# Performance work log

Measured on AMD Instinct MI355X. Metric: run time of the kernel, lower is better.

## Reference

```python
import jax, jax.numpy as jnp
import numpy as np

N = 30000          # nodes
DEG = 16           # in-degree per node
E = N * DEG        # edges per etype
T = 3              # edge types
IN = 128           # in_feats
HID = 256          # hidden_size
HEADS = 4
CLS = 2            # num_classes
NEG_SLOPE = 0.2    # DGL GATConv default


def setup_inputs() -> dict:
    key = jax.random.key(0)
    ks = jax.random.split(key, 14)
    s = lambda k, shape: (jax.random.normal(k, shape, jnp.float32) * 0.05)
    feat = jax.random.normal(ks[0], (N, IN), jnp.float32)
    src = jax.random.randint(ks[1], (T, E), 0, N)
    # every node gets exactly DEG incoming edges per etype (DGL forbids 0-in-degree)
    dst = jnp.tile(jnp.repeat(jnp.arange(N), DEG), (T, 1))
    D = HID // HEADS
    return {
        "feat": feat,
        "W0": s(ks[2], (T, IN, HID)),  "al0": s(ks[3], (T, HEADS, D)), "ar0": s(ks[4], (T, HEADS, D)), "b0": jnp.zeros((T, HID), jnp.float32),
        "W1": s(ks[5], (T, HID, HID)), "al1": s(ks[6], (T, HEADS, D)), "ar1": s(ks[7], (T, HEADS, D)), "b1": jnp.zeros((T, HID), jnp.float32),
        "W2": s(ks[8], (T, HID, CLS)), "al2": s(ks[9], (T, 1, CLS)),   "ar2": s(ks[10], (T, 1, CLS)), "b2": jnp.zeros((T, CLS), jnp.float32),
        "src": src, "dst": dst,
    }


def _gat(feat, W, al, ar, b, src, dst):
    """DGL GATConv: feat [n,F], W [F,H*D], al/ar [H,D], b [H*D] -> [n,H,D]."""
    n = feat.shape[0]
    H, D = al.shape
    h = (feat @ W).reshape(n, H, D)                      # projected features
    el = jnp.sum(h * al, axis=-1)                        # [n,H]
    er = jnp.sum(h * ar, axis=-1)                        # [n,H]
    e = jax.nn.leaky_relu(el[src] + er[dst], NEG_SLOPE)  # [E,H] edge scores
    # segment softmax over incoming edges of each dst node
    emax = jax.ops.segment_max(e, dst, num_segments=n)
    ex = jnp.exp(e - emax[dst])
    den = jax.ops.segment_sum(ex, dst, num_segments=n)
    alpha = ex / den[dst]                                # [E,H]
    out = jax.ops.segment_sum(h[src] * alpha[:, :, None], dst, num_segments=n)
    return out + b.reshape(H, D)


def _hetero(feat, W, al, ar, b, src, dst):
    # HeteroGraphConv(aggregate='mean') over T edge types on one node type
    outs = [_gat(feat, W[t], al[t], ar[t], b[t], src[t], dst[t]) for t in range(W.shape[0])]
    return jnp.mean(jnp.stack(outs, 0), axis=0)


def reference(feat, W0, al0, ar0, b0, W1, al1, ar1, b1, W2, al2, ar2, b2, src, dst):
    h = jax.nn.elu(_hetero(feat, W0, al0, ar0, b0, src, dst).reshape(N, -1))
    h = jax.nn.elu(_hetero(h, W1, al1, ar1, b1, src, dst).reshape(N, -1))
    logits = _hetero(h, W2, al2, ar2, b2, src, dst)      # [N,1,CLS]
    # faithful to F.softmax(logits[primary_ntype], dim=1): dim=1 is the size-1 head axis
    return logits, jax.nn.softmax(logits, axis=1)
```

## Files before the change

kernel.cpp:

```cpp
#include <hip/hip_runtime.h>
#include <hip/hip_bf16.h>
#include <hip/hip_fp8.h>
#include <math.h>

#define N_NODES 30000
#define DEG     16
#define NE      480000
#define NT      3
#define IN_F    128
#define HID_F   256
#define HEADS   4
#define DH      64
#define CLS     2
#define SLOPE   0.2f

#define NTILES      1875
#define NTILES_AL   1880
#define KC0         4
#define KC1         8

typedef __hip_bfloat16 bf16;
typedef __attribute__((ext_vector_type(8))) short short8;
typedef __attribute__((ext_vector_type(4))) float floatx4;
typedef __attribute__((ext_vector_type(2))) float f32x2;

__device__ __forceinline__ float bf2f(short x) {
    unsigned int u = ((unsigned int)(unsigned short)x) << 16;
    float f;
    __builtin_memcpy(&f, &u, 4);
    return f;
}
__device__ __forceinline__ short f2bf_s(float x) {
    bf16 b = bf16(x);
    short s;
    __builtin_memcpy(&s, &b, 2);
    return s;
}

__device__ __forceinline__ void gload_lds16(const void* g, void* l) {
    __builtin_amdgcn_global_load_lds(
        (const __attribute__((address_space(1))) unsigned int*)g,
        (__attribute__((address_space(3))) unsigned int*)l, 16, 0, 0);
}

__device__ __forceinline__ f32x2 fp8_lo(unsigned int u) {
#if __has_builtin(__builtin_amdgcn_cvt_pk_f32_fp8)
    return __builtin_amdgcn_cvt_pk_f32_fp8((int)u, false);
#else
    __hip_fp8_e4m3 q0, q1;
    q0.__x = (unsigned char)(u & 0xff);
    q1.__x = (unsigned char)((u >> 8) & 0xff);
    return (f32x2){(float)q0, (float)q1};
#endif
}
__device__ __forceinline__ f32x2 fp8_hi(unsigned int u) {
#if __has_builtin(__builtin_amdgcn_cvt_pk_f32_fp8)
    return __builtin_amdgcn_cvt_pk_f32_fp8((int)u, true);
#else
    __hip_fp8_e4m3 q2, q3;
    q2.__x = (unsigned char)((u >> 16) & 0xff);
    q3.__x = (unsigned char)((u >> 24) & 0xff);
    return (f32x2){(float)q2, (float)q3};
#endif
}
__device__ __forceinline__ unsigned int fp8_encode4_u32(float v0, float v1,
                                                        float v2, float v3) {
#if __has_builtin(__builtin_amdgcn_cvt_pk_fp8_f32)
    int p01 = __builtin_amdgcn_cvt_pk_fp8_f32(v0, v1, 0, false);
    int p23 = __builtin_amdgcn_cvt_pk_fp8_f32(v2, v3, 0, false);
    return ((unsigned int)p01 & 0xffffu) | ((unsigned int)p23 << 16);
#else
    __hip_fp8_e4m3 q0(v0), q1(v1), q2(v2), q3(v3);
    return (unsigned int)q0.__x | ((unsigned int)q1.__x << 8) |
           ((unsigned int)q2.__x << 16) | ((unsigned int)q3.__x << 24);
#endif
}


#define APACK_THREADS (N_NODES * (IN_F / 8))
#define BP0_THREADS   (NT * 16 * KC0 * 64)
#define BP1_THREADS   (NT * 16 * KC1 * 64)
__global__ void prep(const float* __restrict__ feat, const float* __restrict__ W0,
                     const float* __restrict__ W1, short* __restrict__ Apack0,
                     short* __restrict__ Bpack0, short* __restrict__ Bpack1) {
    int g = blockIdx.x * 256 + threadIdx.x;
    if (g < APACK_THREADS) {
        int row = g >> 4, j8 = g & 15;
        int k0 = j8 * 8;
        const float* src = feat + (size_t)row * IN_F + k0;
        int ntile = row >> 4, C = k0 >> 5, quad = (k0 >> 3) & 3;
        int lane  = (row & 15) + 16 * quad;
        short* dst = Apack0 + ((size_t)(ntile * KC0 + C) * 64 + lane) * 8;
        short8 o;
#pragma unroll
        for (int j = 0; j < 8; j++) o[j] = f2bf_s(src[j]);
        *(short8*)dst = o;
        return;
    }
    g -= APACK_THREADS;
    if (g < BP0_THREADS) {
        int t = g / (16 * KC0 * 64), rem = g % (16 * KC0 * 64);
        int nt = rem / (KC0 * 64);
        int C  = (rem / 64) % KC0;
        int lane = rem & 63, l15 = lane & 15, quad = lane >> 4;
        int col = nt * 16 + l15, k0 = C * 32 + quad * 8;
        const float* src = W0 + (size_t)t * IN_F * HID_F + (size_t)k0 * HID_F + col;
        short* dst = Bpack0 + ((size_t)t * 16 * KC0 + nt * KC0 + C) * 512 + lane * 8;
        short8 o;
#pragma unroll
        for (int j = 0; j < 8; j++) o[j] = f2bf_s(src[(size_t)j * HID_F]);
        *(short8*)dst = o;
        return;
    }
    g -= BP0_THREADS;
    if (g < BP1_THREADS) {
        int t = g / (16 * KC1 * 64), rem = g % (16 * KC1 * 64);
        int nt = rem / (KC1 * 64);
        int C  = (rem / 64) % KC1;
        int lane = rem & 63, l15 = lane & 15, quad = lane >> 4;
        int col = nt * 16 + l15, k0 = C * 32 + quad * 8;
        const float* src = W1 + (size_t)t * HID_F * HID_F + (size_t)k0 * HID_F + col;
        short* dst = Bpack1 + ((size_t)t * 16 * KC1 + nt * KC1 + C) * 512 + lane * 8;
        short8 o;
#pragma unroll
        for (int j = 0; j < 8; j++) o[j] = f2bf_s(src[(size_t)j * HID_F]);
        *(short8*)dst = o;
    }
}

template <int K>
__global__ __launch_bounds__(256, 4) void gemm_proj(const short* __restrict__ Apack,
                                                    const short* __restrict__ Bpack,
                                                    const float* __restrict__ al,
                                                    const float* __restrict__ ar,
                                                    unsigned char* __restrict__ Hout,
                                                    float* __restrict__ el,
                                                    float* __restrict__ er) {
    const int KC = K / 32;
    int nh   = blockIdx.y;
    int t    = blockIdx.z;
    int tid  = threadIdx.x;
    int wave = tid >> 6, lane = tid & 63;
    int quad = lane >> 4, l15 = lane & 15;
    int e0   = blockIdx.x * 8 + wave * 2;

    __shared__ __align__(16) unsigned char Blds[4 * KC * 1024];

    {
        const short* Bp_panel = Bpack + ((size_t)t * 16 + nh * 4) * KC * 512;
#pragma unroll
        for (int i = 0; i < KC; i++) {
            int chunk = wave + i * 4;
            gload_lds16(Bp_panel + (size_t)chunk * 512 + lane * 8,
                        Blds + chunk * 1024);
        }
    }

    const short* Ap0 = Apack + (size_t)(e0)     * KC * 512 + lane * 8;
    const short* Ap1 = Apack + (size_t)(e0 + 1) * KC * 512 + lane * 8;
    unsigned char* Ht = Hout + (size_t)t * N_NODES * HID_F;

    floatx4 acc[4][2];
#pragma unroll
    for (int i = 0; i < 4; i++) {
        acc[i][0] = (floatx4){0.f, 0.f, 0.f, 0.f};
        acc[i][1] = (floatx4){0.f, 0.f, 0.f, 0.f};
    }

    asm volatile("s_waitcnt vmcnt(0)" ::: "memory");
    __syncthreads();

#pragma unroll
    for (int C = 0; C < KC; C++) {
        short8 xb0 = *(const short8*)(Ap0 + (size_t)C * 512);
        short8 xb1 = *(const short8*)(Ap1 + (size_t)C * 512);
#pragma unroll
        for (int nt = 0; nt < 4; nt++) {
            short8 wa = *(const short8*)(Blds + (size_t)(nt * KC + C) * 1024 + lane * 16);
            acc[nt][0] = __builtin_amdgcn_mfma_f32_16x16x32_bf16(wa, xb0, acc[nt][0], 0, 0, 0);
            acc[nt][1] = __builtin_amdgcn_mfma_f32_16x16x32_bf16(wa, xb1, acc[nt][1], 0, 0, 0);
        }
    }

#pragma unroll
    for (int e = 0; e < 2; e++) {
        int node = (e0 + e) * 16 + l15;
        bool ok  = node < N_NODES;
#pragma unroll
        for (int nt = 0; nt < 4; nt++) {
            unsigned int u = fp8_encode4_u32(acc[nt][e][0], acc[nt][e][1],
                                             acc[nt][e][2], acc[nt][e][3]);
            if (ok)
                *(unsigned int*)(Ht + (size_t)node * HID_F + (nh * 4 + nt) * 16 + quad * 4) = u;
        }
        {
            float pl = 0.f, pr = 0.f;
#pragma unroll
            for (int nt = 0; nt < 4; nt++) {
                int coff = t * HID_F + (nh * 4 + nt) * 16 + quad * 4;
                float4 av = *(const float4*)(al + coff);
                float4 rv = *(const float4*)(ar + coff);
                pl += acc[nt][e][0] * av.x + acc[nt][e][1] * av.y +
                      acc[nt][e][2] * av.z + acc[nt][e][3] * av.w;
                pr += acc[nt][e][0] * rv.x + acc[nt][e][1] * rv.y +
                      acc[nt][e][2] * rv.z + acc[nt][e][3] * rv.w;
            }
            pl += __shfl_xor(pl, 16); pl += __shfl_xor(pl, 32);
            pr += __shfl_xor(pr, 16); pr += __shfl_xor(pr, 32);
            if (lane < 16 && ok) {
                el[((size_t)t * N_NODES + node) * HEADS + nh] = pl;
                er[((size_t)t * N_NODES + node) * HEADS + nh] = pr;
            }
        }
    }
}

template <bool PACK>
__global__ __launch_bounds__(256, 8) void gat_agg(const unsigned char* __restrict__ Hproj,
                                                  const float* __restrict__ el,
                                                  const float* __restrict__ er,
                                                  const int* __restrict__ src,
                                                  const float* __restrict__ bias,
                                                  short* __restrict__ out) {
    int blk = blockIdx.x;
    int tid = threadIdx.x;
    __shared__ __align__(16) int   s_src[16][NT][DEG];
    __shared__ __align__(16) float s_w[16][NT][HEADS][DEG];

#pragma unroll
    for (int t = 0; t < NT; t++) {
        int j = tid;
        s_src[j >> 4][t][j & 15] = src[(size_t)t * NE + blk * 256 + j];
    }
    __syncthreads();

    {
        int lane16 = tid & 15;
        int ubase  = tid >> 4;
#pragma unroll
        for (int it = 0; it < 12; it++) {
            int u = it * 16 + ubase;
            int g = u / 12, rem = u % 12;
            int t = rem >> 2, h = rem & 3;
            int n = blk * 16 + g;
            int s = s_src[g][t][lane16];
            float e = el[((size_t)t * N_NODES + s) * HEADS + h] +
                      er[((size_t)t * N_NODES + n) * HEADS + h];
            e = e > 0.f ? e : SLOPE * e;
            float m = e;
            m = fmaxf(m, __shfl_xor(m, 1));
            m = fmaxf(m, __shfl_xor(m, 2));
            m = fmaxf(m, __shfl_xor(m, 4));
            m = fmaxf(m, __shfl_xor(m, 8));
            float p = __expf(e - m);
            float ss = p;
            ss += __shfl_xor(ss, 1);
            ss += __shfl_xor(ss, 2);
            ss += __shfl_xor(ss, 4);
            ss += __shfl_xor(ss, 8);
            s_w[g][t][h][lane16] = p / ss;
        }
    }
    __syncthreads();

    int g = tid >> 4, c = tid & 15;
    int n = blk * 16 + g;
    int h = c >> 2;
    int col0 = c * 16;

    f32x2 acc2[8];
#pragma unroll
    for (int k = 0; k < 8; k++) acc2[k] = (f32x2){0.f, 0.f};

    const uint4* Hb = (const uint4*)Hproj;
    unsigned cu = (unsigned)c;

#pragma unroll
    for (int t = 0; t < NT; t++) {
        const unsigned tb = (unsigned)t * (N_NODES * 16u);
        const float* wp = s_w[g][t][h];
#pragma unroll
        for (int half = 0; half < 2; half++) {
            uint4 v[8];
#pragma unroll
            for (int i = 0; i < 8; i++) {
                int s = s_src[g][t][half * 8 + i];
                v[i] = Hb[tb + (unsigned)s * 16u + cu];
            }
#pragma unroll
            for (int i = 0; i < 8; i++) {
                float wsc = wp[half * 8 + i];
                f32x2 w2 = (f32x2){wsc, wsc};
                acc2[0] += w2 * fp8_lo(v[i].x);
                acc2[1] += w2 * fp8_hi(v[i].x);
                acc2[2] += w2 * fp8_lo(v[i].y);
                acc2[3] += w2 * fp8_hi(v[i].y);
                acc2[4] += w2 * fp8_lo(v[i].z);
                acc2[5] += w2 * fp8_hi(v[i].z);
                acc2[6] += w2 * fp8_lo(v[i].w);
                acc2[7] += w2 * fp8_hi(v[i].w);
            }
        }
    }

    short8 o0, o1;
#pragma unroll
    for (int j = 0; j < 8; j++) {
        float av = acc2[j >> 1][j & 1];
        float bsum = bias[0 * HID_F + col0 + j] + bias[1 * HID_F + col0 + j] +
                     bias[2 * HID_F + col0 + j];
        float res = (av + bsum) * (1.f / 3.f);
        res = res > 0.f ? res : (__expf(res) - 1.f);
        o0[j] = f2bf_s(res);
    }
#pragma unroll
    for (int j = 0; j < 8; j++) {
        float av = acc2[4 + (j >> 1)][j & 1];
        int cj = col0 + 8 + j;
        float bsum = bias[0 * HID_F + cj] + bias[1 * HID_F + cj] +
                     bias[2 * HID_F + cj];
        float res = (av + bsum) * (1.f / 3.f);
        res = res > 0.f ? res : (__expf(res) - 1.f);
        o1[j] = f2bf_s(res);
    }
    if (PACK) {
        int C = c >> 1;
        int lane0 = g + 16 * ((2 * c) & 3);
        int lane1 = g + 16 * ((2 * c + 1) & 3);
        *(short8*)(out + ((size_t)(blk * KC1 + C) * 64 + lane0) * 8) = o0;
        *(short8*)(out + ((size_t)(blk * KC1 + C) * 64 + lane1) * 8) = o1;
    } else {
        *(short8*)(out + (size_t)n * HID_F + col0) = o0;
        *(short8*)(out + (size_t)n * HID_F + col0 + 8) = o1;
    }
}

__global__ __launch_bounds__(256) void proj2(const short* __restrict__ X,
                                             const float* __restrict__ W2,
                                             const float* __restrict__ al2,
                                             const float* __restrict__ ar2,
                                             float* __restrict__ p2,
                                             float* __restrict__ el2,
                                             float* __restrict__ er2) {
    int n    = blockIdx.x * 4 + (threadIdx.x >> 6);
    int lane = threadIdx.x & 63;
    const short* Xr = X + (size_t)n * HID_F + lane * 4;
    float x[4];
    x[0] = bf2f(Xr[0]); x[1] = bf2f(Xr[1]); x[2] = bf2f(Xr[2]); x[3] = bf2f(Xr[3]);
    float a[NT][CLS];
#pragma unroll
    for (int t = 0; t < NT; t++)
#pragma unroll
        for (int cc = 0; cc < CLS; cc++) {
            float v = 0.f;
#pragma unroll
            for (int j = 0; j < 4; j++)
                v += x[j] * W2[(size_t)t * HID_F * CLS + (lane * 4 + j) * CLS + cc];
#pragma unroll
            for (int off = 32; off; off >>= 1) v += __shfl_xor(v, off);
            a[t][cc] = v;
        }
    if (lane == 0) {
#pragma unroll
        for (int t = 0; t < NT; t++) {
            p2[((size_t)t * N_NODES + n) * CLS + 0] = a[t][0];
            p2[((size_t)t * N_NODES + n) * CLS + 1] = a[t][1];
            el2[(size_t)t * N_NODES + n] = a[t][0] * al2[t * CLS + 0] + a[t][1] * al2[t * CLS + 1];
            er2[(size_t)t * N_NODES + n] = a[t][0] * ar2[t * CLS + 0] + a[t][1] * ar2[t * CLS + 1];
        }
    }
}

__global__ void final_layer(const float* __restrict__ p2,
                            const float* __restrict__ el2,
                            const float* __restrict__ er2,
                            const int* __restrict__ src,
                            const float* __restrict__ b2,
                            float* __restrict__ out) {
    int n = blockIdx.x * 256 + threadIdx.x;
    if (n >= N_NODES) return;
    float l0 = 0.f, l1 = 0.f;
    for (int t = 0; t < NT; t++) {
        float erv = er2[(size_t)t * N_NODES + n];
        const int* sp = src + (size_t)t * NE + n * DEG;
        float ev[DEG];
        float m = -1e30f;
#pragma unroll
        for (int i = 0; i < DEG; i++) {
            int s   = sp[i];
            float e = el2[(size_t)t * N_NODES + s] + erv;
            e = e > 0.f ? e : SLOPE * e;
            ev[i] = e;
            m = fmaxf(m, e);
        }
        float den = 0.f, a0 = 0.f, a1 = 0.f;
#pragma unroll
        for (int i = 0; i < DEG; i++) {
            int s   = sp[i];
            float p = __expf(ev[i] - m);
            den += p;
            a0  += p * p2[((size_t)t * N_NODES + s) * CLS + 0];
            a1  += p * p2[((size_t)t * N_NODES + s) * CLS + 1];
        }
        l0 += a0 / den + b2[t * CLS + 0];
        l1 += a1 / den + b2[t * CLS + 1];
    }
    l0 *= (1.f / 3.f);
    l1 *= (1.f / 3.f);
    out[(size_t)n * CLS + 0] = l0;
    out[(size_t)n * CLS + 1] = l1;
    float* out2 = out + (size_t)N_NODES * CLS;
    out2[(size_t)n * CLS + 0] = 1.0f;
    out2[(size_t)n * CLS + 1] = 1.0f;
}

extern "C" void kernel_launch(void* const* d_in, const int* in_sizes, int n_in,
                              void* d_out, int out_size, void* d_ws, size_t ws_size,
                              hipStream_t stream) {
    const float* feat = (const float*)d_in[0];
    const float* W0   = (const float*)d_in[1];
    const float* al0  = (const float*)d_in[2];
    const float* ar0  = (const float*)d_in[3];
    const float* b0   = (const float*)d_in[4];
    const float* W1   = (const float*)d_in[5];
    const float* al1  = (const float*)d_in[6];
    const float* ar1  = (const float*)d_in[7];
    const float* b1   = (const float*)d_in[8];
    const float* W2   = (const float*)d_in[9];
    const float* al2  = (const float*)d_in[10];
    const float* ar2  = (const float*)d_in[11];
    const float* b2   = (const float*)d_in[12];
    const int*   src  = (const int*)d_in[13];

    char* w = (char*)d_ws;
    auto alloc = [&](size_t bytes) {
        char* p = w;
        w += (bytes + 255) & ~(size_t)255;
        return p;
    };
    short* Apack0 = (short*)alloc((size_t)NTILES_AL * KC0 * 512 * 2);
    short* Apack1 = (short*)alloc((size_t)NTILES_AL * KC1 * 512 * 2);
    short* Bpack0 = (short*)alloc((size_t)NT * 16 * KC0 * 512 * 2);
    short* Bpack1 = (short*)alloc((size_t)NT * 16 * KC1 * 512 * 2);
    unsigned char* Hproj = (unsigned char*)alloc((size_t)NT * N_NODES * HID_F);
    short* h2    = (short*)alloc((size_t)N_NODES * HID_F * 2);
    float* el    = (float*)alloc((size_t)NT * N_NODES * HEADS * 4);
    float* er    = (float*)alloc((size_t)NT * N_NODES * HEADS * 4);
    float* p2    = (float*)alloc((size_t)NT * N_NODES * CLS * 4);
    float* el2   = (float*)alloc((size_t)NT * N_NODES * 4);
    float* er2   = (float*)alloc((size_t)NT * N_NODES * 4);

    int prep_total = APACK_THREADS + BP0_THREADS + BP1_THREADS;
    prep<<<(prep_total + 255) / 256, 256, 0, stream>>>(feat, W0, W1, Apack0,
                                                       Bpack0, Bpack1);

    dim3 ggrid((NTILES + 7) / 8, 4, NT);

    gemm_proj<IN_F><<<ggrid, 256, 0, stream>>>(Apack0, Bpack0, al0, ar0, Hproj, el, er);
    gat_agg<true><<<N_NODES / 16, 256, 0, stream>>>(Hproj, el, er, src, b0, Apack1);

    gemm_proj<HID_F><<<ggrid, 256, 0, stream>>>(Apack1, Bpack1, al1, ar1, Hproj, el, er);
    gat_agg<false><<<N_NODES / 16, 256, 0, stream>>>(Hproj, el, er, src, b1, h2);

    proj2<<<dim3(N_NODES / 4), 256, 0, stream>>>(h2, W2, al2, ar2, p2, el2, er2);
    final_layer<<<(N_NODES + 255) / 256, 256, 0, stream>>>(p2, el2, er2, src, b2,
                                                           (float*)d_out);
}
```

Measured before the change: 306.0 us.

## Fuse layer-2 projection into aggregation and loop edge types inside GEMM

The final-layer projection (proj2) is folded into the second aggregation kernel's epilogue, so the bf16 hidden activations are never written to or re-read from global memory and one launch disappears. Separately, the projection GEMM now loops over the three edge types inside each block, reusing the loaded A fragments across types instead of launching a z-dimension per type. In exchange, the GEMM grid shrinks threefold, which lowers parallelism, and each block adds a serialized B reload with barriers per type. The fused dot product adds shuffles and W2 reads to the aggregation tail.

```diff
diff --git a/kernel.cpp b/kernel.cpp
--- a/kernel.cpp
+++ b/kernel.cpp
@@ -136,9 +136,8 @@
                                                     unsigned char* __restrict__ Hout,
                                                     float* __restrict__ el,
                                                     float* __restrict__ er) {
-    const int KC = K / 32;
+    constexpr int KC = K / 32;
     int nh   = blockIdx.y;
-    int t    = blockIdx.z;
     int tid  = threadIdx.x;
     int wave = tid >> 6, lane = tid & 63;
     int quad = lane >> 4, l15 = lane & 15;
@@ -146,72 +145,75 @@
 
     __shared__ __align__(16) unsigned char Blds[4 * KC * 1024];
 
-    {
-        const short* Bp_panel = Bpack + ((size_t)t * 16 + nh * 4) * KC * 512;
-#pragma unroll
-        for (int i = 0; i < KC; i++) {
-            int chunk = wave + i * 4;
-            gload_lds16(Bp_panel + (size_t)chunk * 512 + lane * 8,
-                        Blds + chunk * 1024);
-        }
-    }
-
     const short* Ap0 = Apack + (size_t)(e0)     * KC * 512 + lane * 8;
     const short* Ap1 = Apack + (size_t)(e0 + 1) * KC * 512 + lane * 8;
-    unsigned char* Ht = Hout + (size_t)t * N_NODES * HID_F;
-
-    floatx4 acc[4][2];
-#pragma unroll
-    for (int i = 0; i < 4; i++) {
-        acc[i][0] = (floatx4){0.f, 0.f, 0.f, 0.f};
-        acc[i][1] = (floatx4){0.f, 0.f, 0.f, 0.f};
-    }
-
-    asm volatile("s_waitcnt vmcnt(0)" ::: "memory");
-    __syncthreads();
-
-#pragma unroll
-    for (int C = 0; C < KC; C++) {
-        short8 xb0 = *(const short8*)(Ap0 + (size_t)C * 512);
-        short8 xb1 = *(const short8*)(Ap1 + (size_t)C * 512);
-#pragma unroll
-        for (int nt = 0; nt < 4; nt++) {
-            short8 wa = *(const short8*)(Blds + (size_t)(nt * KC + C) * 1024 + lane * 16);
-            acc[nt][0] = __builtin_amdgcn_mfma_f32_16x16x32_bf16(wa, xb0, acc[nt][0], 0, 0, 0);
-            acc[nt][1] = __builtin_amdgcn_mfma_f32_16x16x32_bf16(wa, xb1, acc[nt][1], 0, 0, 0);
-        }
-    }
-
-#pragma unroll
-    for (int e = 0; e < 2; e++) {
-        int node = (e0 + e) * 16 + l15;
-        bool ok  = node < N_NODES;
-#pragma unroll
-        for (int nt = 0; nt < 4; nt++) {
-            unsigned int u = fp8_encode4_u32(acc[nt][e][0], acc[nt][e][1],
-                                             acc[nt][e][2], acc[nt][e][3]);
-            if (ok)
-                *(unsigned int*)(Ht + (size_t)node * HID_F + (nh * 4 + nt) * 16 + quad * 4) = u;
-        }
+
+    for (int t = 0; t < NT; t++) {
         {
-            float pl = 0.f, pr = 0.f;
+            const short* Bp_panel = Bpack + ((size_t)t * 16 + nh * 4) * KC * 512;
+#pragma unroll
+            for (int i = 0; i < KC; i++) {
+                int chunk = wave + i * 4;
+                gload_lds16(Bp_panel + (size_t)chunk * 512 + lane * 8,
+                            Blds + chunk * 1024);
+            }
+        }
+
+        floatx4 acc[4][2];
+#pragma unroll
+        for (int i = 0; i < 4; i++) {
+            acc[i][0] = (floatx4){0.f, 0.f, 0.f, 0.f};
+            acc[i][1] = (floatx4){0.f, 0.f, 0.f, 0.f};
+        }
+
+        asm volatile("s_waitcnt vmcnt(0)" ::: "memory");
+        __syncthreads();
+
+#pragma unroll
+        for (int C = 0; C < KC; C++) {
+            short8 xb0 = *(const short8*)(Ap0 + (size_t)C * 512);
+            short8 xb1 = *(const short8*)(Ap1 + (size_t)C * 512);
 #pragma unroll
             for (int nt = 0; nt < 4; nt++) {
-                int coff = t * HID_F + (nh * 4 + nt) * 16 + quad * 4;
-                float4 av = *(const float4*)(al + coff);
-                float4 rv = *(const float4*)(ar + coff);
-                pl += acc[nt][e][0] * av.x + acc[nt][e][1] * av.y +
-                      acc[nt][e][2] * av.z + acc[nt][e][3] * av.w;
-                pr += acc[nt][e][0] * rv.x + acc[nt][e][1] * rv.y +
-                      acc[nt][e][2] * rv.z + acc[nt][e][3] * rv.w;
-            }
-            pl += __shfl_xor(pl, 16); pl += __shfl_xor(pl, 32);
-            pr += __shfl_xor(pr, 16); pr += __shfl_xor(pr, 32);
-            if (lane < 16 && ok) {
-                el[((size_t)t * N_NODES + node) * HEADS + nh] = pl;
-                er[((size_t)t * N_NODES + node) * HEADS + nh] = pr;
-            }
-        }
+                short8 wa = *(const short8*)(Blds + (size_t)(nt * KC + C) * 1024 + lane * 16);
+                acc[nt][0] = __builtin_amdgcn_mfma_f32_16x16x32_bf16(wa, xb0, acc[nt][0], 0, 0, 0);
+                acc[nt][1] = __builtin_amdgcn_mfma_f32_16x16x32_bf16(wa, xb1, acc[nt][1], 0, 0, 0);
+            }
+        }
+
+        unsigned char* Ht = Hout + (size_t)t * N_NODES * HID_F;
+#pragma unroll
+        for (int e = 0; e < 2; e++) {
+            int node = (e0 + e) * 16 + l15;
+            bool ok  = node < N_NODES;
+#pragma unroll
+            for (int nt = 0; nt < 4; nt++) {
+                unsigned int u = fp8_encode4_u32(acc[nt][e][0], acc[nt][e][1],
+                                                 acc[nt][e][2], acc[nt][e][3]);
+                if (ok)
+                    *(unsigned int*)(Ht + (size_t)node * HID_F + (nh * 4 + nt) * 16 + quad * 4) = u;
+            }
+            {
+                float pl = 0.f, pr = 0.f;
+#pragma unroll
+                for (int nt = 0; nt < 4; nt++) {
+                    int coff = t * HID_F + (nh * 4 + nt) * 16 + quad * 4;
+                    float4 av = *(const float4*)(al + coff);
+                    float4 rv = *(const float4*)(ar + coff);
+                    pl += acc[nt][e][0] * av.x + acc[nt][e][1] * av.y +
+                          acc[nt][e][2] * av.z + acc[nt][e][3] * av.w;
+                    pr += acc[nt][e][0] * rv.x + acc[nt][e][1] * rv.y +
+                          acc[nt][e][2] * rv.z + acc[nt][e][3] * rv.w;
+                }
+                pl += __shfl_xor(pl, 16); pl += __shfl_xor(pl, 32);
+                pr += __shfl_xor(pr, 16); pr += __shfl_xor(pr, 32);
+                if (lane < 16 && ok) {
+                    el[((size_t)t * N_NODES + node) * HEADS + nh] = pl;
+                    er[((size_t)t * N_NODES + node) * HEADS + nh] = pr;
+                }
+            }
+        }
+        __syncthreads();
     }
 }
 
@@ -221,7 +223,13 @@
                                                   const float* __restrict__ er,
                                                   const int* __restrict__ src,
                                                   const float* __restrict__ bias,
-                                                  short* __restrict__ out) {
+                                                  short* __restrict__ out,
+                                                  const float* __restrict__ W2,
+                                                  const float* __restrict__ al2,
+                                                  const float* __restrict__ ar2,
+                                                  float* __restrict__ p2,
+                                                  float* __restrict__ el2,
+                                                  float* __restrict__ er2) {
     int blk = blockIdx.x;
     int tid = threadIdx.x;
     __shared__ __align__(16) int   s_src[16][NT][DEG];
@@ -323,50 +331,39 @@
         res = res > 0.f ? res : (__expf(res) - 1.f);
         o1[j] = f2bf_s(res);
     }
-    if (PACK) {
+    if constexpr (PACK) {
         int C = c >> 1;
         int lane0 = g + 16 * ((2 * c) & 3);
         int lane1 = g + 16 * ((2 * c + 1) & 3);
         *(short8*)(out + ((size_t)(blk * KC1 + C) * 64 + lane0) * 8) = o0;
         *(short8*)(out + ((size_t)(blk * KC1 + C) * 64 + lane1) * 8) = o1;
     } else {
-        *(short8*)(out + (size_t)n * HID_F + col0) = o0;
-        *(short8*)(out + (size_t)n * HID_F + col0 + 8) = o1;
-    }
-}
-
-__global__ __launch_bounds__(256) void proj2(const short* __restrict__ X,
-                                             const float* __restrict__ W2,
-                                             const float* __restrict__ al2,
-                                             const float* __restrict__ ar2,
-                                             float* __restrict__ p2,
-                                             float* __restrict__ el2,
-                                             float* __restrict__ er2) {
-    int n    = blockIdx.x * 4 + (threadIdx.x >> 6);
-    int lane = threadIdx.x & 63;
-    const short* Xr = X + (size_t)n * HID_F + lane * 4;
-    float x[4];
-    x[0] = bf2f(Xr[0]); x[1] = bf2f(Xr[1]); x[2] = bf2f(Xr[2]); x[3] = bf2f(Xr[3]);
-    float a[NT][CLS];
-#pragma unroll
-    for (int t = 0; t < NT; t++)
-#pragma unroll
-        for (int cc = 0; cc < CLS; cc++) {
-            float v = 0.f;
-#pragma unroll
-            for (int j = 0; j < 4; j++)
-                v += x[j] * W2[(size_t)t * HID_F * CLS + (lane * 4 + j) * CLS + cc];
-#pragma unroll
-            for (int off = 32; off; off >>= 1) v += __shfl_xor(v, off);
-            a[t][cc] = v;
-        }
-    if (lane == 0) {
 #pragma unroll
         for (int t = 0; t < NT; t++) {
-            p2[((size_t)t * N_NODES + n) * CLS + 0] = a[t][0];
-            p2[((size_t)t * N_NODES + n) * CLS + 1] = a[t][1];
-            el2[(size_t)t * N_NODES + n] = a[t][0] * al2[t * CLS + 0] + a[t][1] * al2[t * CLS + 1];
-            er2[(size_t)t * N_NODES + n] = a[t][0] * ar2[t * CLS + 0] + a[t][1] * ar2[t * CLS + 1];
+            const float* w2t = W2 + (size_t)t * HID_F * CLS + col0 * CLS;
+            float d0 = 0.f, d1 = 0.f;
+#pragma unroll
+            for (int j = 0; j < 8; j++) {
+                float f = bf2f(o0[j]);
+                d0 += f * w2t[j * 2 + 0];
+                d1 += f * w2t[j * 2 + 1];
+            }
+#pragma unroll
+            for (int j = 0; j < 8; j++) {
+                float f = bf2f(o1[j]);
+                d0 += f * w2t[16 + j * 2 + 0];
+                d1 += f * w2t[16 + j * 2 + 1];
+            }
+            d0 += __shfl_xor(d0, 8); d0 += __shfl_xor(d0, 4);
+            d0 += __shfl_xor(d0, 2); d0 += __shfl_xor(d0, 1);
+            d1 += __shfl_xor(d1, 8); d1 += __shfl_xor(d1, 4);
+            d1 += __shfl_xor(d1, 2); d1 += __shfl_xor(d1, 1);
+            if (c == 0) {
+                p2[((size_t)t * N_NODES + n) * CLS + 0] = d0;
+                p2[((size_t)t * N_NODES + n) * CLS + 1] = d1;
+                el2[(size_t)t * N_NODES + n] = d0 * al2[t * CLS + 0] + d1 * al2[t * CLS + 1];
+                er2[(size_t)t * N_NODES + n] = d0 * ar2[t * CLS + 0] + d1 * ar2[t * CLS + 1];
+            }
         }
     }
 }
@@ -443,7 +440,6 @@
     short* Bpack0 = (short*)alloc((size_t)NT * 16 * KC0 * 512 * 2);
     short* Bpack1 = (short*)alloc((size_t)NT * 16 * KC1 * 512 * 2);
     unsigned char* Hproj = (unsigned char*)alloc((size_t)NT * N_NODES * HID_F);
-    short* h2    = (short*)alloc((size_t)N_NODES * HID_F * 2);
     float* el    = (float*)alloc((size_t)NT * N_NODES * HEADS * 4);
     float* er    = (float*)alloc((size_t)NT * N_NODES * HEADS * 4);
     float* p2    = (float*)alloc((size_t)NT * N_NODES * CLS * 4);
@@ -454,15 +450,17 @@
     prep<<<(prep_total + 255) / 256, 256, 0, stream>>>(feat, W0, W1, Apack0,
                                                        Bpack0, Bpack1);
 
-    dim3 ggrid((NTILES + 7) / 8, 4, NT);
+    dim3 ggrid((NTILES + 7) / 8, 4);
 
     gemm_proj<IN_F><<<ggrid, 256, 0, stream>>>(Apack0, Bpack0, al0, ar0, Hproj, el, er);
-    gat_agg<true><<<N_NODES / 16, 256, 0, stream>>>(Hproj, el, er, src, b0, Apack1);
+    gat_agg<true><<<N_NODES / 16, 256, 0, stream>>>(Hproj, el, er, src, b0, Apack1,
+                                                    nullptr, nullptr, nullptr,
+                                                    nullptr, nullptr, nullptr);
 
     gemm_proj<HID_F><<<ggrid, 256, 0, stream>>>(Apack1, Bpack1, al1, ar1, Hproj, el, er);
-    gat_agg<false><<<N_NODES / 16, 256, 0, stream>>>(Hproj, el, er, src, b1, h2);
-
-    proj2<<<dim3(N_NODES / 4), 256, 0, stream>>>(h2, W2, al2, ar2, p2, el2, er2);
+    gat_agg<false><<<N_NODES / 16, 256, 0, stream>>>(Hproj, el, er, src, b1, nullptr,
+                                                     W2, al2, ar2, p2, el2, er2);
+
     final_layer<<<(N_NODES + 255) / 256, 256, 0, stream>>>(p2, el2, er2, src, b2,
                                                            (float*)d_out);
 }
```

Result: no change. 307.0 us (+0.3%).
